# Performance work log

Measured on AMD Instinct MI355X. Metric: run time of the kernel, lower is better.

Reference implementation:

```python
import jax, jax.numpy as jnp
import numpy as np


def setup_inputs() -> dict:
    key = jax.random.key(0)
    ks = jax.random.split(key, 8)
    B, QL, CL = 4, 128, 512
    XD, ED, D, YD = 64, 128, 128, 32
    sc = lambda fan_in: 1.0 / np.sqrt(fan_in)
    return {
        "q": jax.random.normal(ks[0], (B, QL, XD), jnp.float32),
        "f_embed": jax.random.normal(ks[1], (B, CL, ED), jnp.float32),
        "att_logits": jax.random.normal(ks[2], (B, QL, CL), jnp.float32),
        "W0": jax.random.normal(ks[3], (XD + ED, D), jnp.float32) * sc(XD + ED),
        "b0": jnp.zeros((D,), jnp.float32),
        "W1": jax.random.normal(ks[4], (D, D), jnp.float32) * sc(D),
        "b1": jnp.zeros((D,), jnp.float32),
        "Wo": jax.random.normal(ks[5], (D, YD), jnp.float32) * sc(D),
        "bo": jnp.zeros((YD,), jnp.float32),
    }


def reference(q, f_embed, att_logits, W0, b0, W1, b1, Wo, bo):
    # MultiInputDense on (qq, ff_embed): concat along last dim -> Dense(relu) x2 -> Dense(y_dim).
    # Split the first matmul so we never materialize the tiled concat:
    # concat([qq, ff]) @ W0 == qq @ W0[:xd] + ff @ W0[xd:]
    xd = q.shape[-1]
    q_part = jnp.einsum('bqx,xd->bqd', q, W0[:xd])          # [B, q_len, dim]
    f_part = jnp.einsum('bce,ed->bcd', f_embed, W0[xd:])    # [B, context_len, dim]
    h = jax.nn.relu(q_part[:, :, None, :] + f_part[:, None, :, :] + b0)  # [B,q,c,dim]
    h = jax.nn.relu(jnp.einsum('bqcd,de->bqce', h, W1) + b1)             # [B,q,c,dim]
    yy_hat = jnp.einsum('bqcd,dy->bqcy', h, Wo) + bo                     # [B,q,c,y_dim]
    att_map = jax.nn.softmax(att_logits, axis=-1)                        # [B,q,c]
    y_hat = jnp.einsum('bqc,bqcy->bqy', att_map, yy_hat)                 # [B,q,y_dim]
    return y_hat
```

## Files before the change

### kernel.cpp

```cpp
#include <hip/hip_runtime.h>

#define B_  4
#define QL  128
#define CL  512
#define XD  64
#define ED  128
#define DD  128
#define YD  32

typedef __attribute__((ext_vector_type(8))) _Float16 f16x8;
typedef __attribute__((ext_vector_type(4))) float f32x4;

__global__ void prep_kernel(const float* __restrict__ qg,
                            const float* __restrict__ fg,
                            const float* __restrict__ W0,
                            const float* __restrict__ b0,
                            const float* __restrict__ W1,
                            _Float16* __restrict__ fph,
                            _Float16* __restrict__ qph,
                            _Float16* __restrict__ w1f) {
  const int bid = blockIdx.x, tid = threadIdx.x;
  __shared__ __align__(16) float fr[128][20];
  __shared__ float w1s[32][65];

  if (bid < 128) {
    const int r0 = bid * 16;
    #pragma unroll
    for (int i = 0; i < 8; ++i) {
      int idx = i * 256 + tid;
      fr[idx & 127][idx >> 7] = fg[((size_t)r0 + (idx >> 7)) * ED + (idx & 127)];
    }
    __syncthreads();
    const int d = tid & 127, half = tid >> 7;
    float acc[8] = {};
    const float* w = W0 + XD * DD + d;
    for (int e = 0; e < ED; ++e) {
      float wv = w[e * DD];
      f32x4 f0 = *(const f32x4*)&fr[e][half * 8];
      f32x4 f1 = *(const f32x4*)&fr[e][half * 8 + 4];
      #pragma unroll
      for (int j = 0; j < 4; ++j) {
        acc[j]     = fmaf(f0[j], wv, acc[j]);
        acc[j + 4] = fmaf(f1[j], wv, acc[j + 4]);
      }
    }
    const int kk = d >> 5, lhi = (d >> 3) & 3, e2 = d & 7;
    #pragma unroll
    for (int j = 0; j < 8; ++j) {
      int R = r0 + half * 8 + j;
      int b = R >> 9, c = R & 511;
      int t = c >> 7, cc = c & 127;
      int chunk = ((b * 4 + t) * 4 + kk) * 8 + (cc >> 6) * 4 + ((cc >> 4) & 3);
      fph[((size_t)chunk << 9) + ((size_t)(lhi * 16 + (cc & 15)) << 3) + e2] = (_Float16)acc[j];
    }
  } else if (bid < 160) {
    const int r0 = (bid - 128) * 16;
    #pragma unroll
    for (int i = 0; i < 4; ++i) {
      int idx = i * 256 + tid;
      fr[idx & 63][idx >> 6] = qg[((size_t)r0 + (idx >> 6)) * XD + (idx & 63)];
    }
    __syncthreads();
    const int d = tid & 127, half = tid >> 7;
    float acc[8];
    float bv = b0[d];
    #pragma unroll
    for (int j = 0; j < 8; ++j) acc[j] = bv;
    const float* w = W0 + d;
    for (int e = 0; e < XD; ++e) {
      float wv = w[e * DD];
      f32x4 f0 = *(const f32x4*)&fr[e][half * 8];
      f32x4 f1 = *(const f32x4*)&fr[e][half * 8 + 4];
      #pragma unroll
      for (int j = 0; j < 4; ++j) {
        acc[j]     = fmaf(f0[j], wv, acc[j]);
        acc[j + 4] = fmaf(f1[j], wv, acc[j + 4]);
      }
    }
    #pragma unroll
    for (int j = 0; j < 8; ++j)
      qph[((size_t)r0 + half * 8 + j) * DD + d] = (_Float16)acc[j];
  } else {
    const int id8 = bid - 160;
    const int wcol = id8 & 1, kk = id8 >> 1;
    #pragma unroll
    for (int i = 0; i < 8; ++i) {
      int idx = i * 256 + tid;
      w1s[idx >> 6][idx & 63] = W1[(kk * 32 + (idx >> 6)) * DD + wcol * 64 + (idx & 63)];
    }
    __syncthreads();
    const int jt = tid >> 6, ln = tid & 63;
    const int llo = ln & 15, lhi = ln >> 4;
    f16x8 v;
    #pragma unroll
    for (int e = 0; e < 8; ++e)
      v[e] = (_Float16)w1s[lhi * 8 + e][jt * 16 + llo];
    *(f16x8*)(w1f + ((((size_t)wcol * 4 + kk) * 4 + jt) * 64 + ln) * 8) = v;
  }
}

__launch_bounds__(256, 2)
__global__ void main_kernel(const float* __restrict__ logits,
                            const _Float16* __restrict__ fph,
                            const _Float16* __restrict__ qph,
                            const _Float16* __restrict__ w1f,
                            const float* __restrict__ b1,
                            const float* __restrict__ Wo,
                            const float* __restrict__ bo,
                            float* __restrict__ out) {
  __shared__ __align__(16) float att[CL];
  __shared__ float g[4][DD];
  __shared__ float red[8];
  __shared__ float part[8][YD];

  const int tid = threadIdx.x;
  const int bid = blockIdx.x;
  const int wid = tid >> 6, ln = tid & 63;
  const int b = bid >> 7;
  const int wrow = wid >> 1, wcol = wid & 1;
  const int lhi = ln >> 4, llo = ln & 15;

  ((float*)g)[tid] = 0.f;
  ((float*)g)[tid + 256] = 0.f;

  f16x8 wf[4][4];
  {
    const uint4* ws = (const uint4*)w1f;
    #pragma unroll
    for (int kk = 0; kk < 4; ++kk)
      #pragma unroll
      for (int jt = 0; jt < 4; ++jt) {
        uint4 u = ws[(((wcol * 4 + kk) * 4 + jt) << 6) + ln];
        wf[kk][jt] = *(const f16x8*)&u;
      }
  }
  f16x8 qpv[4];
  {
    const uint4* qs = (const uint4*)(qph + (size_t)bid * DD);
    #pragma unroll
    for (int kk = 0; kk < 4; ++kk) {
      uint4 u = qs[(kk * 32 + lhi * 8) >> 3];
      qpv[kk] = *(const f16x8*)&u;
    }
  }

  {
    const float* lgr = logits + (size_t)bid * CL;
    float l0 = lgr[tid], l1 = lgr[tid + 256];
    float m = fmaxf(l0, l1);
    #pragma unroll
    for (int off = 1; off < 64; off <<= 1) m = fmaxf(m, __shfl_xor(m, off, 64));
    if (ln == 0) red[wid] = m;
    __syncthreads();
    m = fmaxf(fmaxf(red[0], red[1]), fmaxf(red[2], red[3]));
    float p0 = expf(l0 - m), p1 = expf(l1 - m);
    float s = p0 + p1;
    #pragma unroll
    for (int off = 1; off < 64; off <<= 1) s += __shfl_xor(s, off, 64);
    if (ln == 0) red[4 + wid] = s;
    __syncthreads();
    float inv = 1.f / (red[4] + red[5] + red[6] + red[7]);
    att[tid] = p0 * inv;
    att[tid + 256] = p1 * inv;
  }
  __syncthreads();

  const int j0 = wcol * 64 + llo;
  float b1v[4];
  #pragma unroll
  for (int jt = 0; jt < 4; ++jt) b1v[jt] = b1[j0 + jt * 16];

  float gp[4] = {0.f, 0.f, 0.f, 0.f};
  const f16x8 zf = {};
  const uint4* fpv = (const uint4*)fph;

  #pragma unroll
  for (int t = 0; t < 4; ++t) {
    f32x4 acc[4][4];
    #pragma unroll
    for (int ct = 0; ct < 4; ++ct)
      #pragma unroll
      for (int jt = 0; jt < 4; ++jt)
        acc[ct][jt] = (f32x4){b1v[jt], b1v[jt], b1v[jt], b1v[jt]};

    #pragma unroll
    for (int kk = 0; kk < 4; ++kk) {
      const int cb = ((((b * 4 + t) * 4 + kk) * 8 + wrow * 4) << 6);
      f16x8 a[4];
      #pragma unroll
      for (int ct = 0; ct < 4; ++ct) {
        uint4 u = fpv[cb + (ct << 6) + ln];
        f16x8 x = *(const f16x8*)&u + qpv[kk];
        a[ct] = __builtin_elementwise_max(x, zf);
      }
      #pragma unroll
      for (int ct = 0; ct < 4; ++ct)
        #pragma unroll
        for (int jt = 0; jt < 4; ++jt)
          acc[ct][jt] = __builtin_amdgcn_mfma_f32_16x16x32_f16(a[ct], wf[kk][jt], acc[ct][jt], 0, 0, 0);
    }

    const int cbase = t * 128 + wrow * 64 + lhi * 4;
    #pragma unroll
    for (int ct = 0; ct < 4; ++ct) {
      f32x4 a4 = *(const f32x4*)&att[cbase + ct * 16];
      #pragma unroll
      for (int r = 0; r < 4; ++r)
        #pragma unroll
        for (int jt = 0; jt < 4; ++jt)
          gp[jt] = fmaf(a4[r], fmaxf(acc[ct][jt][r], 0.f), gp[jt]);
    }
  }

  #pragma unroll
  for (int jt = 0; jt < 4; ++jt) {
    gp[jt] += __shfl_xor(gp[jt], 16, 64);
    gp[jt] += __shfl_xor(gp[jt], 32, 64);
  }
  __syncthreads();
  if (ln < 16) {
    #pragma unroll
    for (int jt = 0; jt < 4; ++jt) g[wid][j0 + jt * 16] = gp[jt];
  }
  __syncthreads();

  {
    int y = tid & 31, ch = tid >> 5;
    float a = 0.f;
    #pragma unroll
    for (int jj = 0; jj < 16; ++jj) {
      int j = ch * 16 + jj;
      float gj = g[0][j] + g[1][j] + g[2][j] + g[3][j];
      a = fmaf(gj, Wo[j * YD + y], a);
    }
    part[ch][y] = a;
  }
  __syncthreads();
  if (tid < YD) {
    float a = bo[tid];
    #pragma unroll
    for (int ch = 0; ch < 8; ++ch) a += part[ch][tid];
    out[(size_t)bid * YD + tid] = a;
  }
}

extern "C" void kernel_launch(void* const* d_in, const int* in_sizes, int n_in,
                              void* d_out, int out_size, void* d_ws, size_t ws_size,
                              hipStream_t stream) {
  const float* q  = (const float*)d_in[0];
  const float* f  = (const float*)d_in[1];
  const float* lg = (const float*)d_in[2];
  const float* W0 = (const float*)d_in[3];
  const float* b0 = (const float*)d_in[4];
  const float* W1 = (const float*)d_in[5];
  const float* b1 = (const float*)d_in[6];
  const float* Wo = (const float*)d_in[7];
  const float* bo = (const float*)d_in[8];
  float* out = (float*)d_out;

  _Float16* fph = (_Float16*)d_ws;
  _Float16* qph = fph + (size_t)512 * 512;
  _Float16* w1f = qph + (size_t)B_ * QL * DD;

  prep_kernel<<<168, 256, 0, stream>>>(q, f, W0, b0, W1, fph, qph, w1f);
  main_kernel<<<B_ * QL, 256, 0, stream>>>(lg, fph, qph, w1f, b1, Wo, bo, out);
}
```

Baseline: 23.85 us.

## Spread context tiles across sixteen waves and stage W1 fragments in LDS

Each block grows from 256 to 1024 threads. Each of the 16 waves now handles one context tile `t` instead of looping over four, which removes the serial t-loop per wave. W1 fragments are copied once into shared memory and read from there, instead of being held in registers for the whole kernel. The cost is a larger cross-wave reduction over 16 partial sums, plus a `__launch_bounds__(1024, 4)` hint that may force a very low VGPR budget and cause register spills.

```diff
diff --git a/kernel.cpp b/kernel.cpp
--- a/kernel.cpp
+++ b/kernel.cpp
@@ -99,7 +99,7 @@
   }
 }
 
-__launch_bounds__(256, 2)
+__launch_bounds__(1024, 4)
 __global__ void main_kernel(const float* __restrict__ logits,
                             const _Float16* __restrict__ fph,
                             const _Float16* __restrict__ qph,
@@ -108,130 +108,129 @@
                             const float* __restrict__ Wo,
                             const float* __restrict__ bo,
                             float* __restrict__ out) {
+  __shared__ __align__(16) _Float16 wls[16384];
   __shared__ __align__(16) float att[CL];
-  __shared__ float g[4][DD];
-  __shared__ float red[8];
+  __shared__ float g[16][DD];
+  __shared__ float gsum[DD];
+  __shared__ float red[16];
   __shared__ float part[8][YD];
 
   const int tid = threadIdx.x;
   const int bid = blockIdx.x;
   const int wid = tid >> 6, ln = tid & 63;
   const int b = bid >> 7;
-  const int wrow = wid >> 1, wcol = wid & 1;
+  const int t = wid >> 2, wrow = (wid >> 1) & 1, wcol = wid & 1;
   const int lhi = ln >> 4, llo = ln & 15;
 
+  {
+    const uint4* src = (const uint4*)w1f;
+    uint4* dst = (uint4*)wls;
+    dst[tid] = src[tid];
+    dst[tid + 1024] = src[tid + 1024];
+  }
   ((float*)g)[tid] = 0.f;
-  ((float*)g)[tid + 256] = 0.f;
-
-  f16x8 wf[4][4];
-  {
-    const uint4* ws = (const uint4*)w1f;
-    #pragma unroll
-    for (int kk = 0; kk < 4; ++kk)
-      #pragma unroll
-      for (int jt = 0; jt < 4; ++jt) {
-        uint4 u = ws[(((wcol * 4 + kk) * 4 + jt) << 6) + ln];
-        wf[kk][jt] = *(const f16x8*)&u;
-      }
-  }
-  f16x8 qpv[4];
-  {
-    const uint4* qs = (const uint4*)(qph + (size_t)bid * DD);
-    #pragma unroll
-    for (int kk = 0; kk < 4; ++kk) {
-      uint4 u = qs[(kk * 32 + lhi * 8) >> 3];
-      qpv[kk] = *(const f16x8*)&u;
-    }
-  }
-
-  {
-    const float* lgr = logits + (size_t)bid * CL;
-    float l0 = lgr[tid], l1 = lgr[tid + 256];
-    float m = fmaxf(l0, l1);
+  ((float*)g)[tid + 1024] = 0.f;
+
+  float sm_l = 0.f;
+  if (tid < 512) {
+    sm_l = logits[(size_t)bid * CL + tid];
+    float m = sm_l;
     #pragma unroll
     for (int off = 1; off < 64; off <<= 1) m = fmaxf(m, __shfl_xor(m, off, 64));
     if (ln == 0) red[wid] = m;
-    __syncthreads();
-    m = fmaxf(fmaxf(red[0], red[1]), fmaxf(red[2], red[3]));
-    float p0 = expf(l0 - m), p1 = expf(l1 - m);
-    float s = p0 + p1;
+  }
+  __syncthreads();
+  if (tid < 512) {
+    float m = red[0];
+    #pragma unroll
+    for (int w = 1; w < 8; ++w) m = fmaxf(m, red[w]);
+    float p = expf(sm_l - m);
+    float s = p;
     #pragma unroll
     for (int off = 1; off < 64; off <<= 1) s += __shfl_xor(s, off, 64);
-    if (ln == 0) red[4 + wid] = s;
-    __syncthreads();
-    float inv = 1.f / (red[4] + red[5] + red[6] + red[7]);
-    att[tid] = p0 * inv;
-    att[tid + 256] = p1 * inv;
-  }
-  __syncthreads();
-
-  const int j0 = wcol * 64 + llo;
+    if (ln == 0) red[8 + wid] = s;
+    sm_l = p;
+  }
+  __syncthreads();
+  if (tid < 512) {
+    float tot = red[8];
+    #pragma unroll
+    for (int w = 9; w < 16; ++w) tot += red[w];
+    att[tid] = sm_l / tot;
+  }
+  __syncthreads();
+
   float b1v[4];
   #pragma unroll
-  for (int jt = 0; jt < 4; ++jt) b1v[jt] = b1[j0 + jt * 16];
+  for (int jt = 0; jt < 4; ++jt) b1v[jt] = b1[wcol * 64 + jt * 16 + llo];
+
+  f32x4 acc[4][4];
+  #pragma unroll
+  for (int ct = 0; ct < 4; ++ct)
+    #pragma unroll
+    for (int jt = 0; jt < 4; ++jt)
+      acc[ct][jt] = (f32x4){b1v[jt], b1v[jt], b1v[jt], b1v[jt]};
+
+  const uint4* fpv = (const uint4*)fph;
+  const _Float16* qrow = qph + (size_t)bid * DD;
+  const f16x8 zf = {};
+
+  #pragma unroll
+  for (int kk = 0; kk < 4; ++kk) {
+    const f16x8 qk = *(const f16x8*)(qrow + kk * 32 + lhi * 8);
+    f16x8 a[4];
+    #pragma unroll
+    for (int ct = 0; ct < 4; ++ct) {
+      const int chunk = ((b * 4 + t) * 4 + kk) * 8 + wrow * 4 + ct;
+      uint4 u = fpv[chunk * 64 + ln];
+      f16x8 x = *(const f16x8*)&u + qk;
+      a[ct] = __builtin_elementwise_max(x, zf);
+    }
+    #pragma unroll
+    for (int jt = 0; jt < 4; ++jt) {
+      f16x8 wv = *(const f16x8*)(wls + (size_t)((((wcol * 4 + kk) * 4 + jt) * 64 + ln) * 8));
+      #pragma unroll
+      for (int ct = 0; ct < 4; ++ct)
+        acc[ct][jt] = __builtin_amdgcn_mfma_f32_16x16x32_f16(a[ct], wv, acc[ct][jt], 0, 0, 0);
+    }
+  }
 
   float gp[4] = {0.f, 0.f, 0.f, 0.f};
-  const f16x8 zf = {};
-  const uint4* fpv = (const uint4*)fph;
-
-  #pragma unroll
-  for (int t = 0; t < 4; ++t) {
-    f32x4 acc[4][4];
-    #pragma unroll
-    for (int ct = 0; ct < 4; ++ct)
+  const int cb = t * 128 + wrow * 64 + lhi * 4;
+  #pragma unroll
+  for (int ct = 0; ct < 4; ++ct) {
+    f32x4 a4 = *(const f32x4*)&att[cb + ct * 16];
+    #pragma unroll
+    for (int r = 0; r < 4; ++r)
       #pragma unroll
       for (int jt = 0; jt < 4; ++jt)
-        acc[ct][jt] = (f32x4){b1v[jt], b1v[jt], b1v[jt], b1v[jt]};
-
-    #pragma unroll
-    for (int kk = 0; kk < 4; ++kk) {
-      const int cb = ((((b * 4 + t) * 4 + kk) * 8 + wrow * 4) << 6);
-      f16x8 a[4];
-      #pragma unroll
-      for (int ct = 0; ct < 4; ++ct) {
-        uint4 u = fpv[cb + (ct << 6) + ln];
-        f16x8 x = *(const f16x8*)&u + qpv[kk];
-        a[ct] = __builtin_elementwise_max(x, zf);
-      }
-      #pragma unroll
-      for (int ct = 0; ct < 4; ++ct)
-        #pragma unroll
-        for (int jt = 0; jt < 4; ++jt)
-          acc[ct][jt] = __builtin_amdgcn_mfma_f32_16x16x32_f16(a[ct], wf[kk][jt], acc[ct][jt], 0, 0, 0);
-    }
-
-    const int cbase = t * 128 + wrow * 64 + lhi * 4;
-    #pragma unroll
-    for (int ct = 0; ct < 4; ++ct) {
-      f32x4 a4 = *(const f32x4*)&att[cbase + ct * 16];
-      #pragma unroll
-      for (int r = 0; r < 4; ++r)
-        #pragma unroll
-        for (int jt = 0; jt < 4; ++jt)
-          gp[jt] = fmaf(a4[r], fmaxf(acc[ct][jt][r], 0.f), gp[jt]);
-    }
-  }
-
+        gp[jt] = fmaf(a4[r], fmaxf(acc[ct][jt][r], 0.f), gp[jt]);
+  }
   #pragma unroll
   for (int jt = 0; jt < 4; ++jt) {
     gp[jt] += __shfl_xor(gp[jt], 16, 64);
     gp[jt] += __shfl_xor(gp[jt], 32, 64);
   }
-  __syncthreads();
   if (ln < 16) {
     #pragma unroll
-    for (int jt = 0; jt < 4; ++jt) g[wid][j0 + jt * 16] = gp[jt];
-  }
-  __syncthreads();
-
-  {
-    int y = tid & 31, ch = tid >> 5;
+    for (int jt = 0; jt < 4; ++jt) g[wid][wcol * 64 + jt * 16 + ln] = gp[jt];
+  }
+  __syncthreads();
+
+  if (tid < 128) {
+    float s = 0.f;
+    #pragma unroll
+    for (int w = 0; w < 16; ++w) s += g[w][tid];
+    gsum[tid] = s;
+  }
+  __syncthreads();
+  if (tid < 256) {
+    const int ch = tid >> 5, y = tid & 31;
     float a = 0.f;
     #pragma unroll
     for (int jj = 0; jj < 16; ++jj) {
       int j = ch * 16 + jj;
-      float gj = g[0][j] + g[1][j] + g[2][j] + g[3][j];
-      a = fmaf(gj, Wo[j * YD + y], a);
+      a = fmaf(gsum[j], Wo[j * YD + y], a);
     }
     part[ch][y] = a;
   }
@@ -263,5 +262,5 @@
   _Float16* w1f = qph + (size_t)B_ * QL * DD;
 
   prep_kernel<<<168, 256, 0, stream>>>(q, f, W0, b0, W1, fph, qph, w1f);
-  main_kernel<<<B_ * QL, 256, 0, stream>>>(lg, fph, qph, w1f, b1, Wo, bo, out);
+  main_kernel<<<B_ * QL, 1024, 0, stream>>>(lg, fph, qph, w1f, b1, Wo, bo, out);
 }
```

After: 28.50 us. 19.5% more time.
